# Optimization experiments

Hardware: AMD Instinct MI355X
Metric: run time of the kernel (lower is better)

## Reference

```python
import jax, jax.numpy as jnp
import numpy as np

B, ND, NK = 4096, 32, 64        # batch, num_drones, num_docks
FD, FK = 16, 16                  # nfeat_drone, nfeat_dock
NHID, H = 128, 4                 # hidden dim, attention heads
ALPHA = 0.2                      # leaky relu slope
NEG = -9e15                      # masking constant from torch code


def setup_inputs() -> dict:
    key = jax.random.key(0)
    ks = jax.random.split(key, 13)
    s = 0.1
    obs = jax.random.normal(ks[0], (B, ND * FD + NK * FK + ND * NK), jnp.float32)
    return {
        "obs": obs,
        # DroneDockGAT params (per-head projections + additive attention vectors)
        "W_drone": jax.random.normal(ks[1], (H, FD, NHID), jnp.float32) * s,
        "W_dock": jax.random.normal(ks[2], (H, FK, NHID), jnp.float32) * s,
        "a_src": jax.random.normal(ks[3], (H, NHID), jnp.float32) * s,
        "a_dst": jax.random.normal(ks[4], (H, NHID), jnp.float32) * s,
        # critic: Linear(nhid*num_drones,64) -> ReLU -> Linear(64,1)
        "Wc1": jax.random.normal(ks[5], (NHID * ND, 64), jnp.float32) * s,
        "bc1": jnp.zeros((64,), jnp.float32),
        "Wc2": jax.random.normal(ks[6], (64, 1), jnp.float32) * s,
        "bc2": jnp.zeros((1,), jnp.float32),
        # actor heads
        "Wad": jax.random.normal(ks[7], (NHID, NHID), jnp.float32) * s,
        "bad": jnp.zeros((NHID,), jnp.float32),
        "Wak": jax.random.normal(ks[8], (NHID, NHID), jnp.float32) * s,
        "bak": jnp.zeros((NHID,), jnp.float32),
    }


def reference(obs, W_drone, W_dock, a_src, a_dst, Wc1, bc1, Wc2, bc2, Wad, bad, Wak, bak):
    sd, sk = ND * FD, NK * FK
    drone = obs[:, :sd].reshape(B, ND, FD)
    dock = obs[:, sd:sd + sk].reshape(B, NK, FK)
    adj = obs[:, sd + sk:].reshape(B, ND, NK)

    # per-head projections: [B, H, ND, NHID] / [B, H, NK, NHID]
    Whd = jnp.einsum('bnf,hfk->bhnk', drone, W_drone)
    Whk = jnp.einsum('bmf,hfk->bhmk', dock, W_dock)

    # additive GAT attention scores e[b,h,n,m]
    e = jax.nn.leaky_relu(
        jnp.einsum('bhnk,hk->bhn', Whd, a_src)[:, :, :, None]
        + jnp.einsum('bhmk,hk->bhm', Whk, a_dst)[:, :, None, :],
        ALPHA,
    )
    e = jnp.where(adj[:, None, :, :] > 0, e, NEG)
    attn = jax.nn.softmax(e, axis=-1)

    # head-averaged outputs with ELU
    h_drone = jax.nn.elu(jnp.einsum('bhnm,bhmk->bnk', attn, Whk) / H)  # [B, ND, NHID]
    h_dock = jax.nn.elu(Whk.mean(axis=1))                               # [B, NK, NHID]

    # critic
    values = jax.nn.relu(h_drone.reshape(B, -1) @ Wc1 + bc1) @ Wc2 + bc2  # [B, 1]

    # actor: masked drone-dock score matrix
    q = h_drone @ Wad + bad
    k = h_dock @ Wak + bak
    scores = jnp.einsum('bnk,bmk->bnm', q, k)
    logits = jnp.where(adj > 0, scores, NEG)  # [B, ND, NK]
    return values, logits
```

## Files before the change

kernel.cpp:

```cpp
#include <hip/hip_runtime.h>
#include <math.h>

#define OBSD 3584
#define NEGC -9e15f

typedef short short8 __attribute__((ext_vector_type(8)));
typedef float float4v __attribute__((ext_vector_type(4)));

#define WS_MT_S   0
#define WS_U_F    8192
#define WS_W_F    8320
#define WS_C0_F   8448
#define WS_AW_F   8452
#define WS_WDMT_S 17160
#define WS_WFT_S  19208
#define WS_WC1H_S 32768
#define WS_WC1L_S 294912
#define WS_HD_S   557056
#define WS_NEED_BYTES  1114112ull
#define WS_NEED2_BYTES 34668544ull

__device__ __forceinline__ float elu_f(float x) {
    return x > 0.f ? x : (__expf(x) - 1.f);
}
__device__ __forceinline__ short f2bf(float f) {
    union { float f; unsigned u; } v; v.f = f;
    unsigned u = v.u;
    unsigned r = (u + 0x7fffu + ((u >> 16) & 1u)) >> 16;
    return (short)r;
}
__device__ __forceinline__ float b2f(short s) {
    union { unsigned u; float f; } v; v.u = ((unsigned)(unsigned short)s) << 16;
    return v.f;
}
__device__ __forceinline__ unsigned pk2(float a, float b) {
    return (unsigned)(unsigned short)f2bf(a) | ((unsigned)(unsigned short)f2bf(b) << 16);
}

__global__ __launch_bounds__(256) void setup_fold(
    const float* __restrict__ W_drone, const float* __restrict__ W_dock,
    const float* __restrict__ a_src, const float* __restrict__ a_dst,
    const float* __restrict__ Wad, const float* __restrict__ Wak,
    const float* __restrict__ bad, const float* __restrict__ bak,
    float* __restrict__ wsf, short* __restrict__ wss)
{
    const int t = threadIdx.x, bi = blockIdx.x;
    if (bi < 16) {
        __shared__ float sa[32 * 132];
        __shared__ float sb[32 * 132];
        const int r0 = (bi >> 2) * 32, i0 = (bi & 3) * 32;
        #pragma unroll
        for (int qq = 0; qq < 4; ++qq) {
            int e = (t + 256 * qq) * 4;
            int r = e >> 7, cc = e & 127;
            *(float4*)&sa[r * 132 + cc] = *(const float4*)&Wad[(r0 + r) * 128 + cc];
            *(float4*)&sb[r * 132 + cc] = *(const float4*)&Wak[(i0 + r) * 128 + cc];
        }
        __syncthreads();
        int rr = (t >> 4) * 2, ii = (t & 15) * 2;
        float a00 = 0.f, a01 = 0.f, a10 = 0.f, a11 = 0.f;
        for (int c = 0; c < 128; ++c) {
            float x0 = sa[rr * 132 + c], x1 = sa[(rr + 1) * 132 + c];
            float y0 = sb[ii * 132 + c], y1 = sb[(ii + 1) * 132 + c];
            a00 += x0 * y0; a01 += x0 * y1; a10 += x1 * y0; a11 += x1 * y1;
        }
        wss[WS_MT_S + (i0 + ii) * 128 + (r0 + rr)]         = f2bf(a00);
        wss[WS_MT_S + (i0 + ii + 1) * 128 + (r0 + rr)]     = f2bf(a01);
        wss[WS_MT_S + (i0 + ii) * 128 + (r0 + rr + 1)]     = f2bf(a10);
        wss[WS_MT_S + (i0 + ii + 1) * 128 + (r0 + rr + 1)] = f2bf(a11);
    } else if (bi == 16) {
        if (t < 128) {
            float acc = 0.f;
            for (int c = 0; c < 128; ++c) acc += Wad[t * 128 + c] * bak[c];
            wsf[WS_U_F + t] = acc;
        } else {
            int j = t - 128;
            float acc = 0.f;
            for (int c = 0; c < 128; ++c) acc += Wak[j * 128 + c] * bad[c];
            wsf[WS_W_F + j] = acc;
        }
        if (t == 0) {
            float acc = 0.f;
            for (int c = 0; c < 128; ++c) acc += bad[c] * bak[c];
            wsf[WS_C0_F] = acc;
        }
    } else {
        if (t < 64) {
            int h = t >> 4, f = t & 15;
            const float* wrow = W_drone + h * 2048 + f * 128;
            const float* arow = a_src + h * 128;
            float acc = 0.f;
            for (int k = 0; k < 128; ++k) acc += wrow[k] * arow[k];
            wsf[WS_AW_F + t] = acc;
        } else if (t < 128) {
            int tt = t - 64;
            int h = tt >> 4, f = tt & 15;
            const float* wrow = W_dock + h * 2048 + f * 128;
            const float* arow = a_dst + h * 128;
            float acc = 0.f;
            for (int k = 0; k < 128; ++k) acc += wrow[k] * arow[k];
            wsf[WS_AW_F + 64 + tt] = acc;
        }
        for (int idx = t; idx < 2048; idx += 256) {
            int k2 = idx >> 4, f = idx & 15;
            float v = 0.25f * (W_dock[f * 128 + k2] + W_dock[2048 + f * 128 + k2]
                             + W_dock[4096 + f * 128 + k2] + W_dock[6144 + f * 128 + k2]);
            wss[WS_WDMT_S + k2 * 16 + f] = f2bf(v);
        }
        for (int idx = t; idx < 8192; idx += 256) {
            int k2 = idx >> 6, f64 = idx & 63;
            float v = W_dock[(f64 >> 4) * 2048 + (f64 & 15) * 128 + k2];
            wss[WS_WFT_S + k2 * 64 + f64] = f2bf(v);
        }
    }
}

__global__ __launch_bounds__(256) void setup_wc1(
    const float* __restrict__ Wc1,
    short* __restrict__ wc1h, short* __restrict__ wc1l)
{
    __shared__ float tile[64 * 68];
    const int t = threadIdx.x;
    const int k0 = blockIdx.x * 64;
    {
        int r = t >> 2, c0 = (t & 3) * 16;
        const float4* src = (const float4*)&Wc1[(size_t)(k0 + r) * 64 + c0];
        #pragma unroll
        for (int u = 0; u < 4; ++u)
            *(float4*)&tile[r * 68 + c0 + 4 * u] = src[u];
    }
    __syncthreads();
    {
        int col = t >> 2, kk0 = (t & 3) * 16;
        short hi[16], lo[16];
        #pragma unroll
        for (int j = 0; j < 16; ++j) {
            float v = tile[(kk0 + j) * 68 + col];
            hi[j] = f2bf(v);
            lo[j] = f2bf(v - b2f(hi[j]));
        }
        uint4* dh = (uint4*)(wc1h + (size_t)col * 4096 + k0 + kk0);
        uint4* dl = (uint4*)(wc1l + (size_t)col * 4096 + k0 + kk0);
        dh[0] = *(uint4*)&hi[0]; dh[1] = *(uint4*)&hi[8];
        dl[0] = *(uint4*)&lo[0]; dl[1] = *(uint4*)&lo[8];
    }
}

__global__ __launch_bounds__(256, 2) void k13_fused(
    const float* __restrict__ obs,
    const float* __restrict__ wsf, const short* __restrict__ wss,
    short* __restrict__ hdg,
    float* __restrict__ out_logits)
{
    __shared__ __align__(16) char sm[74240];
    short* sD     = (short*)(sm + 0);
    short* sK     = (short*)(sm + 1024);
    short* sAdj   = (short*)(sm + 3072);
    float* sAw    = (float*)(sm + 7680);
    float* sSrc   = (float*)(sm + 8192);
    float* sDst   = (float*)(sm + 8704);
    short* sAt    = (short*)(sm + 9728);
    short* sT     = (short*)(sm + 28160);
    short* sHd    = (short*)(sm + 32768);
    short* sWf    = (short*)(sm + 41472);
    short* dockRm = (short*)(sm + 0);
    float* suL    = (float*)(sm + 8192);
    float* swL    = (float*)(sm + 8320);
    float* uL     = (float*)(sm + 8704);
    float* wL     = (float*)(sm + 9216);
    short* hkS    = (short*)(sm + 9728);
    short* wdmTS  = (short*)(sm + 28160);
    short* t2S    = (short*)(sm + 32768);
    short* MtS    = (short*)(sm + 41472);

    const int t = threadIdx.x;
    const int b = blockIdx.x;
    const float* obsrow = obs + (size_t)b * OBSD;
    const int L = t & 63, c = L & 15, q = L >> 4, w = t >> 6;

    #pragma unroll
    for (int i = 0; i < 4; ++i) {
        int q4 = t + 256 * i;
        if (q4 < 896) {
            float4 v = ((const float4*)obsrow)[q4];
            int e0 = q4 * 4;
            if (e0 < 512) {
                int n = e0 >> 4, f0 = e0 & 15;
                sD[(f0 + 0) * 32 + n] = f2bf(v.x);
                sD[(f0 + 1) * 32 + n] = f2bf(v.y);
                sD[(f0 + 2) * 32 + n] = f2bf(v.z);
                sD[(f0 + 3) * 32 + n] = f2bf(v.w);
            } else if (e0 < 1536) {
                int e = e0 - 512;
                int m = e >> 4, f0 = e & 15;
                sK[(f0 + 0) * 64 + m] = f2bf(v.x);
                sK[(f0 + 1) * 64 + m] = f2bf(v.y);
                sK[(f0 + 2) * 64 + m] = f2bf(v.z);
                sK[(f0 + 3) * 64 + m] = f2bf(v.w);
            } else {
                int e = e0 - 1536;
                int n = e >> 6, m0 = e & 63;
                uint2 pkd = { pk2(v.x, v.y), pk2(v.z, v.w) };
                *(uint2*)&sAdj[n * 72 + m0] = pkd;
            }
        }
    }
    #pragma unroll
    for (int i = 0; i < 4; ++i)
        ((uint4*)sWf)[t + 256 * i] = ((const uint4*)(wss + WS_WFT_S))[t + 256 * i];
    if (t < 128) sAw[t] = wsf[WS_AW_F + t];
    __syncthreads();

    if (t < 128) {
        int h = t >> 5, n = t & 31;
        float acc = 0.f;
        #pragma unroll
        for (int f = 0; f < 16; ++f) acc += b2f(sD[f * 32 + n]) * sAw[h * 16 + f];
        sSrc[h * 32 + n] = acc;
    }
    {
        int h = t >> 6, m = t & 63;
        float acc = 0.f;
        #pragma unroll
        for (int f = 0; f < 16; ++f) acc += b2f(sK[f * 64 + m]) * sAw[64 + h * 16 + f];
        sDst[h * 64 + m] = acc;
    }
    __syncthreads();

    {
        int row = t >> 1, j = t & 1;
        int h = row >> 5, n = row & 31, m0 = j * 32;
        float sv = sSrc[h * 32 + n];
        float e32[32];
        float pmax = -INFINITY;
        #pragma unroll
        for (int mm = 0; mm < 32; ++mm) {
            int m = m0 + mm;
            float e = sv + sDst[h * 64 + m];
            e = e > 0.f ? e : 0.2f * e;
            e = (b2f(sAdj[n * 72 + m]) > 0.f) ? e : NEGC;
            e32[mm] = e;
            pmax = fmaxf(pmax, e);
        }
        pmax = fmaxf(pmax, __shfl_xor(pmax, 1, 2));
        float psum = 0.f;
        #pragma unroll
        for (int mm = 0; mm < 32; ++mm) { e32[mm] = __expf(e32[mm] - pmax); psum += e32[mm]; }
        psum += __shfl_xor(psum, 1, 2);
        float rinv = 1.f / psum;
        unsigned* ab = (unsigned*)sAt;
        int ub = (h * 2304 + n * 72 + m0) >> 1;
        #pragma unroll
        for (int mm = 0; mm < 32; mm += 2)
            ab[ub + (mm >> 1)] = pk2(e32[mm] * rinv, e32[mm + 1] * rinv);
    }
    __syncthreads();

    {
        int h = w;
        float4v accT[2] = { {0,0,0,0}, {0,0,0,0} };
        #pragma unroll
        for (int mt = 0; mt < 2; ++mt)
            #pragma unroll
            for (int kq = 0; kq < 2; ++kq) {
                short8 a = *(const short8*)&sAt[h * 2304 + (mt * 16 + c) * 72 + kq * 32 + q * 8];
                short8 bb = *(const short8*)&sK[c * 64 + kq * 32 + q * 8];
                accT[mt] = __builtin_amdgcn_mfma_f32_16x16x32_bf16(a, bb, accT[mt], 0, 0, 0);
            }
        #pragma unroll
        for (int mt = 0; mt < 2; ++mt)
            #pragma unroll
            for (int i = 0; i < 4; ++i)
                sT[(mt * 16 + q * 4 + i) * 72 + h * 16 + c] = f2bf(accT[mt][i]);
    }
    __syncthreads();

    {
        int mt = w & 1, ntb = (w >> 1) * 4;
        float4v acc[4] = { {0,0,0,0}, {0,0,0,0}, {0,0,0,0}, {0,0,0,0} };
        #pragma unroll
        for (int kq = 0; kq < 2; ++kq) {
            short8 a = *(const short8*)&sT[(mt * 16 + c) * 72 + kq * 32 + q * 8];
            #pragma unroll
            for (int p = 0; p < 4; ++p) {
                short8 bb = *(const short8*)&sWf[((ntb + p) * 16 + c) * 64 + kq * 32 + q * 8];
                acc[p] = __builtin_amdgcn_mfma_f32_16x16x32_bf16(a, bb, acc[p], 0, 0, 0);
            }
        }
        #pragma unroll
        for (int p = 0; p < 4; ++p)
            #pragma unroll
            for (int i = 0; i < 4; ++i) {
                float v = elu_f(acc[p][i] * 0.25f);
                sHd[(mt * 16 + q * 4 + i) * 136 + (ntb + p) * 16 + c] = f2bf(v);
            }
    }
    __syncthreads();

    {
        int n = t >> 3, k2 = (t & 7) * 16;
        uint4 x0 = *(const uint4*)&sHd[n * 136 + k2];
        uint4 x1 = *(const uint4*)&sHd[n * 136 + k2 + 8];
        uint4* dst = (uint4*)(hdg + (size_t)b * 4096 + n * 128 + k2);
        dst[0] = x0; dst[1] = x1;
    }
    {
        float4 v = ((const float4*)obsrow)[128 + t];
        int m = t >> 2, f0 = (t & 3) * 4;
        uint2 pkd = { pk2(v.x, v.y), pk2(v.z, v.w) };
        *(uint2*)&dockRm[m * 16 + f0] = pkd;
    }
    ((uint4*)wdmTS)[t] = ((const uint4*)(wss + WS_WDMT_S))[t];
    #pragma unroll
    for (int i = 0; i < 8; ++i)
        ((uint4*)MtS)[t + 256 * i] = ((const uint4*)(wss + WS_MT_S))[t + 256 * i];
    if (t < 128) uL[t] = wsf[WS_U_F + t];
    else wL[t - 128] = wsf[WS_W_F + (t - 128)];
    __syncthreads();

    {
        int mt = w;
        short8 a;
        if (q < 2) a = *(const short8*)&dockRm[(mt * 16 + c) * 16 + q * 8];
        else a = short8{0, 0, 0, 0, 0, 0, 0, 0};
        float swp[4] = {0.f, 0.f, 0.f, 0.f};
        #pragma unroll
        for (int nt = 0; nt < 8; ++nt) {
            short8 bb;
            if (q < 2) bb = *(const short8*)&wdmTS[(nt * 16 + c) * 16 + q * 8];
            else bb = short8{0, 0, 0, 0, 0, 0, 0, 0};
            float4v acc = {0, 0, 0, 0};
            acc = __builtin_amdgcn_mfma_f32_16x16x32_bf16(a, bb, acc, 0, 0, 0);
            float wv = wL[nt * 16 + c];
            #pragma unroll
            for (int i = 0; i < 4; ++i) {
                float ev = elu_f(acc[i]);
                hkS[(mt * 16 + q * 4 + i) * 136 + nt * 16 + c] = f2bf(ev);
                swp[i] += ev * wv;
            }
        }
        #pragma unroll
        for (int i = 0; i < 4; ++i) {
            float sv = swp[i];
            sv += __shfl_xor(sv, 1, 16);
            sv += __shfl_xor(sv, 2, 16);
            sv += __shfl_xor(sv, 4, 16);
            sv += __shfl_xor(sv, 8, 16);
            if (c == 0) swL[mt * 16 + q * 4 + i] = sv;
        }
    }
    {
        int n = t >> 3, p = t & 7;
        float a = 0.f;
        #pragma unroll
        for (int kk = 0; kk < 16; kk += 2) {
            unsigned uu = *(const unsigned*)&sHd[n * 136 + p * 16 + kk];
            a += b2f((short)(uu & 0xffff)) * uL[p * 16 + kk]
               + b2f((short)(uu >> 16))   * uL[p * 16 + kk + 1];
        }
        a += __shfl_xor(a, 1, 8);
        a += __shfl_xor(a, 2, 8);
        a += __shfl_xor(a, 4, 8);
        if (p == 0) suL[n] = a;
    }
    __syncthreads();

    {
        int mt = w & 1, ntb = (w >> 1) * 4;
        float4v acc[4] = { {0,0,0,0}, {0,0,0,0}, {0,0,0,0}, {0,0,0,0} };
        #pragma unroll
        for (int kq = 0; kq < 4; ++kq) {
            short8 a = *(const short8*)&sHd[(mt * 16 + c) * 136 + kq * 32 + q * 8];
            #pragma unroll
            for (int p = 0; p < 4; ++p) {
                short8 bb = *(const short8*)&MtS[((ntb + p) * 16 + c) * 128 + kq * 32 + q * 8];
                acc[p] = __builtin_amdgcn_mfma_f32_16x16x32_bf16(a, bb, acc[p], 0, 0, 0);
            }
        }
        __syncthreads();
        #pragma unroll
        for (int p = 0; p < 4; ++p)
            #pragma unroll
            for (int i = 0; i < 4; ++i)
                t2S[(mt * 16 + q * 4 + i) * 136 + (ntb + p) * 16 + c] = f2bf(acc[p][i]);
    }
    __syncthreads();

    {
        const float c0v = wsf[WS_C0_F];
        int ntd = w;
        float* lg = out_logits + (size_t)b * 2048;
        #pragma unroll
        for (int mt = 0; mt < 2; ++mt) {
            float4v acc = {0, 0, 0, 0};
            #pragma unroll
            for (int kq = 0; kq < 4; ++kq) {
                short8 a  = *(const short8*)&t2S[(mt * 16 + c) * 136 + kq * 32 + q * 8];
                short8 bb = *(const short8*)&hkS[(ntd * 16 + c) * 136 + kq * 32 + q * 8];
                acc = __builtin_amdgcn_mfma_f32_16x16x32_bf16(a, bb, acc, 0, 0, 0);
            }
            int col = ntd * 16 + c;
            float swv = swL[col];
            #pragma unroll
            for (int i = 0; i < 4; ++i) {
                int row = mt * 16 + q * 4 + i;
                float val = acc[i] + suL[row] + swv + c0v;
                bool keep = b2f(sAdj[row * 72 + col]) > 0.f;
                lg[row * 64 + col] = keep ? val : NEGC;
            }
        }
    }
}

__global__ __launch_bounds__(256, 2) void k1_attn_hd(
    const float* __restrict__ obs,
    const float* __restrict__ wsf, const short* __restrict__ wss,
    short* __restrict__ hdg)
{
    __shared__ __align__(16) char sm[57856];
    short* sD   = (short*)(sm + 0);
    short* sK   = (short*)(sm + 1024);
    short* sAdj = (short*)(sm + 3072);
    float* sAw  = (float*)(sm + 7680);
    float* sSrc = (float*)(sm + 8192);
    float* sDst = (float*)(sm + 8704);
    short* sAt  = (short*)(sm + 9728);
    short* sT   = (short*)(sm + 28160);
    short* sHd  = (short*)(sm + 32768);
    short* sWf  = (short*)(sm + 41472);

    const int t = threadIdx.x;
    const int b = blockIdx.x;
    const float* obsrow = obs + (size_t)b * OBSD;
    const int L = t & 63, c = L & 15, q = L >> 4, w = t >> 6;

    #pragma unroll
    for (int i = 0; i < 4; ++i) {
        int q4 = t + 256 * i;
        if (q4 < 896) {
            float4 v = ((const float4*)obsrow)[q4];
            int e0 = q4 * 4;
            if (e0 < 512) {
                int n = e0 >> 4, f0 = e0 & 15;
                sD[(f0 + 0) * 32 + n] = f2bf(v.x);
                sD[(f0 + 1) * 32 + n] = f2bf(v.y);
                sD[(f0 + 2) * 32 + n] = f2bf(v.z);
                sD[(f0 + 3) * 32 + n] = f2bf(v.w);
            } else if (e0 < 1536) {
                int e = e0 - 512;
                int m = e >> 4, f0 = e & 15;
                sK[(f0 + 0) * 64 + m] = f2bf(v.x);
                sK[(f0 + 1) * 64 + m] = f2bf(v.y);
                sK[(f0 + 2) * 64 + m] = f2bf(v.z);
                sK[(f0 + 3) * 64 + m] = f2bf(v.w);
            } else {
                int e = e0 - 1536;
                int n = e >> 6, m0 = e & 63;
                uint2 pkd = { pk2(v.x, v.y), pk2(v.z, v.w) };
                *(uint2*)&sAdj[n * 72 + m0] = pkd;
            }
        }
    }
    #pragma unroll
    for (int i = 0; i < 4; ++i)
        ((uint4*)sWf)[t + 256 * i] = ((const uint4*)(wss + WS_WFT_S))[t + 256 * i];
    if (t < 128) sAw[t] = wsf[WS_AW_F + t];
    __syncthreads();

    if (t < 128) {
        int h = t >> 5, n = t & 31;
        float acc = 0.f;
        #pragma unroll
        for (int f = 0; f < 16; ++f) acc += b2f(sD[f * 32 + n]) * sAw[h * 16 + f];
        sSrc[h * 32 + n] = acc;
    }
    {
        int h = t >> 6, m = t & 63;
        float acc = 0.f;
        #pragma unroll
        for (int f = 0; f < 16; ++f) acc += b2f(sK[f * 64 + m]) * sAw[64 + h * 16 + f];
        sDst[h * 64 + m] = acc;
    }
    __syncthreads();

    {
        int row = t >> 1, j = t & 1;
        int h = row >> 5, n = row & 31, m0 = j * 32;
        float sv = sSrc[h * 32 + n];
        float e32[32];
        float pmax = -INFINITY;
        #pragma unroll
        for (int mm = 0; mm < 32; ++mm) {
            int m = m0 + mm;
            float e = sv + sDst[h * 64 + m];
            e = e > 0.f ? e : 0.2f * e;
            e = (b2f(sAdj[n * 72 + m]) > 0.f) ? e : NEGC;
            e32[mm] = e;
            pmax = fmaxf(pmax, e);
        }
        pmax = fmaxf(pmax, __shfl_xor(pmax, 1, 2));
        float psum = 0.f;
        #pragma unroll
        for (int mm = 0; mm < 32; ++mm) { e32[mm] = __expf(e32[mm] - pmax); psum += e32[mm]; }
        psum += __shfl_xor(psum, 1, 2);
        float rinv = 1.f / psum;
        unsigned* ab = (unsigned*)sAt;
        int ub = (h * 2304 + n * 72 + m0) >> 1;
        #pragma unroll
        for (int mm = 0; mm < 32; mm += 2)
            ab[ub + (mm >> 1)] = pk2(e32[mm] * rinv, e32[mm + 1] * rinv);
    }
    __syncthreads();

    {
        int h = w;
        float4v accT[2] = { {0,0,0,0}, {0,0,0,0} };
        #pragma unroll
        for (int mt = 0; mt < 2; ++mt)
            #pragma unroll
            for (int kq = 0; kq < 2; ++kq) {
                short8 a = *(const short8*)&sAt[h * 2304 + (mt * 16 + c) * 72 + kq * 32 + q * 8];
                short8 bb = *(const short8*)&sK[c * 64 + kq * 32 + q * 8];
                accT[mt] = __builtin_amdgcn_mfma_f32_16x16x32_bf16(a, bb, accT[mt], 0, 0, 0);
            }
        #pragma unroll
        for (int mt = 0; mt < 2; ++mt)
            #pragma unroll
            for (int i = 0; i < 4; ++i)
                sT[(mt * 16 + q * 4 + i) * 72 + h * 16 + c] = f2bf(accT[mt][i]);
    }
    __syncthreads();

    {
        int mt = w & 1, ntb = (w >> 1) * 4;
        float4v acc[4] = { {0,0,0,0}, {0,0,0,0}, {0,0,0,0}, {0,0,0,0} };
        #pragma unroll
        for (int kq = 0; kq < 2; ++kq) {
            short8 a = *(const short8*)&sT[(mt * 16 + c) * 72 + kq * 32 + q * 8];
            #pragma unroll
            for (int p = 0; p < 4; ++p) {
                short8 bb = *(const short8*)&sWf[((ntb + p) * 16 + c) * 64 + kq * 32 + q * 8];
                acc[p] = __builtin_amdgcn_mfma_f32_16x16x32_bf16(a, bb, acc[p], 0, 0, 0);
            }
        }
        #pragma unroll
        for (int p = 0; p < 4; ++p)
            #pragma unroll
            for (int i = 0; i < 4; ++i) {
                float v = elu_f(acc[p][i] * 0.25f);
                sHd[(mt * 16 + q * 4 + i) * 136 + (ntb + p) * 16 + c] = f2bf(v);
            }
    }
    __syncthreads();

    {
        int n = t >> 3, k2 = (t & 7) * 16;
        uint4 x0 = *(const uint4*)&sHd[n * 136 + k2];
        uint4 x1 = *(const uint4*)&sHd[n * 136 + k2 + 8];
        uint4* dst = (uint4*)(hdg + (size_t)b * 4096 + n * 128 + k2);
        dst[0] = x0; dst[1] = x1;
    }
}

__global__ __launch_bounds__(256) void k2_critic(
    const short* __restrict__ hdg,
    const float* __restrict__ Wc1, const float* __restrict__ bc1,
    const float* __restrict__ Wc2, const float* __restrict__ bc2,
    float* __restrict__ out_values)
{
    __shared__ __align__(16) char sm[46592];
    short* As   = (short*)(sm + 0);
    float* Wst  = (float*)(sm + 9216);
    short* Bh   = (short*)(sm + 27648);
    short* Blo  = (short*)(sm + 36864);
    float* bc1L = (float*)(sm + 46080);
    float* wc2L = (float*)(sm + 46336);

    const int t = threadIdx.x;
    const int r0 = blockIdx.x * 64;
    const int L = t & 63, c = L & 15, q = L >> 4, w = t >> 6;

    if (t < 64) { bc1L[t] = bc1[t]; wc2L[t] = Wc2[t]; }

    float4v acc[4] = { {0,0,0,0}, {0,0,0,0}, {0,0,0,0}, {0,0,0,0} };

    for (int kc = 0; kc < 64; ++kc) {
        __syncthreads();
        {
            int r = t >> 2, kk0 = (t & 3) * 16;
            const uint4* src = (const uint4*)(hdg + (size_t)(r0 + r) * 4096 + kc * 64 + kk0);
            *(uint4*)&As[r * 72 + kk0]     = src[0];
            *(uint4*)&As[r * 72 + kk0 + 8] = src[1];
        }
        {
            int el = t >> 2, j0 = (t & 3) * 16;
            const float4* src = (const float4*)&Wc1[(size_t)(kc * 64 + el) * 64 + j0];
            #pragma unroll
            for (int u = 0; u < 4; ++u)
                *(float4*)&Wst[el * 72 + j0 + 4 * u] = src[u];
        }
        __syncthreads();
        {
            int j = t & 63, elb = (t >> 6) * 16;
            #pragma unroll
            for (int e = 0; e < 16; e += 2) {
                float v0 = Wst[(elb + e) * 72 + j];
                float v1 = Wst[(elb + e + 1) * 72 + j];
                short h0 = f2bf(v0), h1 = f2bf(v1);
                float l0 = v0 - b2f(h0), l1 = v1 - b2f(h1);
                *(unsigned*)&Bh[j * 72 + elb + e]  = (unsigned)(unsigned short)h0 | ((unsigned)(unsigned short)h1 << 16);
                *(unsigned*)&Blo[j * 72 + elb + e] = (unsigned)(unsigned short)f2bf(l0) | ((unsigned)(unsigned short)f2bf(l1) << 16);
            }
        }
        __syncthreads();
        #pragma unroll
        for (int kq = 0; kq < 2; ++kq) {
            short8 a = *(const short8*)&As[(w * 16 + c) * 72 + kq * 32 + q * 8];
            #pragma unroll
            for (int ct = 0; ct < 4; ++ct) {
                short8 bh = *(const short8*)&Bh[(ct * 16 + c) * 72 + kq * 32 + q * 8];
                short8 bl = *(const short8*)&Blo[(ct * 16 + c) * 72 + kq * 32 + q * 8];
                acc[ct] = __builtin_amdgcn_mfma_f32_16x16x32_bf16(a, bh, acc[ct], 0, 0, 0);
                acc[ct] = __builtin_amdgcn_mfma_f32_16x16x32_bf16(a, bl, acc[ct], 0, 0, 0);
            }
        }
    }
    float bc2v = bc2[0];
    #pragma unroll
    for (int i = 0; i < 4; ++i) {
        float sv = 0.f;
        #pragma unroll
        for (int ct = 0; ct < 4; ++ct) {
            float pre = acc[ct][i] + bc1L[ct * 16 + c];
            pre = fmaxf(pre, 0.f);
            sv += pre * wc2L[ct * 16 + c];
        }
        sv += __shfl_xor(sv, 1, 16);
        sv += __shfl_xor(sv, 2, 16);
        sv += __shfl_xor(sv, 4, 16);
        sv += __shfl_xor(sv, 8, 16);
        if (c == 0) out_values[r0 + w * 16 + q * 4 + i] = sv + bc2v;
    }
}

__global__ __launch_bounds__(256) void k2_critic2(
    const short* __restrict__ hdg,
    const short* __restrict__ wc1h, const short* __restrict__ wc1l,
    const float* __restrict__ bc1,
    const float* __restrict__ Wc2, const float* __restrict__ bc2,
    float* __restrict__ out_values)
{
    __shared__ __align__(16) char sm[39936];
    short* As   = (short*)(sm + 0);
    short* Bh   = (short*)(sm + 4352);
    short* Bl   = (short*)(sm + 21760);
    float* bc1L = (float*)(sm + 39168);
    float* wc2L = (float*)(sm + 39424);
    float* red  = (float*)(sm + 39680);

    const int t = threadIdx.x;
    const int r0 = blockIdx.x * 16;
    const int L = t & 63, c = L & 15, q = L >> 4, w = t >> 6;

    if (t < 64) { bc1L[t] = bc1[t]; wc2L[t] = Wc2[t]; }

    float4v acc = {0, 0, 0, 0};

    const int rA  = t >> 4,  kkA = (t & 15) * 8;
    const int colB = t >> 2, kbB = (t & 3) * 32;

    for (int it = 0; it < 32; ++it) {
        const int kc = it * 128;
        __syncthreads();
        *(uint4*)&As[rA * 136 + kkA] =
            *(const uint4*)(hdg + (size_t)(r0 + rA) * 4096 + kc + kkA);
        {
            const uint4* srcH = (const uint4*)(wc1h + (size_t)colB * 4096 + kc + kbB);
            const uint4* srcL = (const uint4*)(wc1l + (size_t)colB * 4096 + kc + kbB);
            #pragma unroll
            for (int u = 0; u < 4; ++u) {
                *(uint4*)&Bh[colB * 136 + kbB + 8 * u] = srcH[u];
                *(uint4*)&Bl[colB * 136 + kbB + 8 * u] = srcL[u];
            }
        }
        __syncthreads();
        #pragma unroll
        for (int kq = 0; kq < 4; ++kq) {
            short8 a  = *(const short8*)&As[c * 136 + kq * 32 + q * 8];
            short8 bh = *(const short8*)&Bh[(w * 16 + c) * 136 + kq * 32 + q * 8];
            short8 bl = *(const short8*)&Bl[(w * 16 + c) * 136 + kq * 32 + q * 8];
            acc = __builtin_amdgcn_mfma_f32_16x16x32_bf16(a, bh, acc, 0, 0, 0);
            acc = __builtin_amdgcn_mfma_f32_16x16x32_bf16(a, bl, acc, 0, 0, 0);
        }
    }
    #pragma unroll
    for (int i = 0; i < 4; ++i) {
        float pre = acc[i] + bc1L[w * 16 + c];
        pre = fmaxf(pre, 0.f);
        float sv = pre * wc2L[w * 16 + c];
        sv += __shfl_xor(sv, 1, 16);
        sv += __shfl_xor(sv, 2, 16);
        sv += __shfl_xor(sv, 4, 16);
        sv += __shfl_xor(sv, 8, 16);
        if (c == 0) red[w * 16 + q * 4 + i] = sv;
    }
    __syncthreads();
    if (t < 16) {
        float v = red[t] + red[16 + t] + red[32 + t] + red[48 + t] + bc2[0];
        out_values[r0 + t] = v;
    }
}

__global__ __launch_bounds__(256, 2) void k3_logits(
    const float* __restrict__ obs,
    const float* __restrict__ wsf, const short* __restrict__ wss,
    float* __restrict__ out_logits)
{
    __shared__ __align__(16) char sm[75648];
    short* dockRm = (short*)(sm + 0);
    short* adjBf  = (short*)(sm + 2048);
    short* hdS    = (short*)(sm + 6656);
    short* hkS    = (short*)(sm + 15360);
    short* wdmTS  = (short*)(sm + 32768);
    short* t2S    = (short*)(sm + 32768);
    float* suL    = (float*)(sm + 41472);
    float* swL    = (float*)(sm + 41600);
    float* uL     = (float*)(sm + 41856);
    float* wL     = (float*)(sm + 42368);
    short* MtS    = (short*)(sm + 42880);

    const int t = threadIdx.x;
    const int b = blockIdx.x;
    const float* obsrow = obs + (size_t)b * OBSD;
    short* hdg = (short*)out_logits;
    const int L = t & 63, c = L & 15, q = L >> 4, w = t >> 6;

    {
        int n = t >> 3, k2 = (t & 7) * 16;
        const uint4* src = (const uint4*)(hdg + (size_t)b * 4096 + n * 128 + k2);
        uint4 x0 = src[0], x1 = src[1];
        *(uint4*)&hdS[n * 136 + k2]     = x0;
        *(uint4*)&hdS[n * 136 + k2 + 8] = x1;
    }
    {
        float4 v = ((const float4*)obsrow)[128 + t];
        int m = t >> 2, f0 = (t & 3) * 4;
        uint2 pkd = { pk2(v.x, v.y), pk2(v.z, v.w) };
        *(uint2*)&dockRm[m * 16 + f0] = pkd;
    }
    #pragma unroll
    for (int i = 0; i < 2; ++i) {
        int q4 = 384 + t + 256 * i;
        if (q4 < 896) {
            float4 v = ((const float4*)obsrow)[q4];
            int e = q4 * 4 - 1536;
            int n = e >> 6, m0 = e & 63;
            uint2 pkd = { pk2(v.x, v.y), pk2(v.z, v.w) };
            *(uint2*)&adjBf[n * 72 + m0] = pkd;
        }
    }
    ((uint4*)wdmTS)[t] = ((const uint4*)(wss + WS_WDMT_S))[t];
    #pragma unroll
    for (int i = 0; i < 8; ++i)
        ((uint4*)MtS)[t + 256 * i] = ((const uint4*)(wss + WS_MT_S))[t + 256 * i];
    if (t < 128) uL[t] = wsf[WS_U_F + t];
    else wL[t - 128] = wsf[WS_W_F + (t - 128)];
    __syncthreads();

    {
        int mt = w;
        short8 a;
        if (q < 2) a = *(const short8*)&dockRm[(mt * 16 + c) * 16 + q * 8];
        else a = short8{0, 0, 0, 0, 0, 0, 0, 0};
        float swp[4] = {0.f, 0.f, 0.f, 0.f};
        #pragma unroll
        for (int nt = 0; nt < 8; ++nt) {
            short8 bb;
            if (q < 2) bb = *(const short8*)&wdmTS[(nt * 16 + c) * 16 + q * 8];
            else bb = short8{0, 0, 0, 0, 0, 0, 0, 0};
            float4v acc = {0, 0, 0, 0};
            acc = __builtin_amdgcn_mfma_f32_16x16x32_bf16(a, bb, acc, 0, 0, 0);
            float wv = wL[nt * 16 + c];
            #pragma unroll
            for (int i = 0; i < 4; ++i) {
                float ev = elu_f(acc[i]);
                hkS[(mt * 16 + q * 4 + i) * 136 + nt * 16 + c] = f2bf(ev);
                swp[i] += ev * wv;
            }
        }
        #pragma unroll
        for (int i = 0; i < 4; ++i) {
            float sv = swp[i];
            sv += __shfl_xor(sv, 1, 16);
            sv += __shfl_xor(sv, 2, 16);
            sv += __shfl_xor(sv, 4, 16);
            sv += __shfl_xor(sv, 8, 16);
            if (c == 0) swL[mt * 16 + q * 4 + i] = sv;
        }
    }
    {
        int n = t >> 3, p = t & 7;
        float a = 0.f;
        #pragma unroll
        for (int kk = 0; kk < 16; kk += 2) {
            unsigned uu = *(const unsigned*)&hdS[n * 136 + p * 16 + kk];
            a += b2f((short)(uu & 0xffff)) * uL[p * 16 + kk]
               + b2f((short)(uu >> 16))   * uL[p * 16 + kk + 1];
        }
        a += __shfl_xor(a, 1, 8);
        a += __shfl_xor(a, 2, 8);
        a += __shfl_xor(a, 4, 8);
        if (p == 0) suL[n] = a;
    }
    __syncthreads();

    {
        int mt = w & 1, ntb = (w >> 1) * 4;
        float4v acc[4] = { {0,0,0,0}, {0,0,0,0}, {0,0,0,0}, {0,0,0,0} };
        #pragma unroll
        for (int kq = 0; kq < 4; ++kq) {
            short8 a = *(const short8*)&hdS[(mt * 16 + c) * 136 + kq * 32 + q * 8];
            #pragma unroll
            for (int p = 0; p < 4; ++p) {
                short8 bb = *(const short8*)&MtS[((ntb + p) * 16 + c) * 128 + kq * 32 + q * 8];
                acc[p] = __builtin_amdgcn_mfma_f32_16x16x32_bf16(a, bb, acc[p], 0, 0, 0);
            }
        }
        __syncthreads();
        #pragma unroll
        for (int p = 0; p < 4; ++p)
            #pragma unroll
            for (int i = 0; i < 4; ++i)
                t2S[(mt * 16 + q * 4 + i) * 136 + (ntb + p) * 16 + c] = f2bf(acc[p][i]);
    }
    __syncthreads();

    {
        const float c0v = wsf[WS_C0_F];
        int ntd = w;
        float* lg = out_logits + (size_t)b * 2048;
        #pragma unroll
        for (int mt = 0; mt < 2; ++mt) {
            float4v acc = {0, 0, 0, 0};
            #pragma unroll
            for (int kq = 0; kq < 4; ++kq) {
                short8 a  = *(const short8*)&t2S[(mt * 16 + c) * 136 + kq * 32 + q * 8];
                short8 bb = *(const short8*)&hkS[(ntd * 16 + c) * 136 + kq * 32 + q * 8];
                acc = __builtin_amdgcn_mfma_f32_16x16x32_bf16(a, bb, acc, 0, 0, 0);
            }
            int col = ntd * 16 + c;
            float swv = swL[col];
            #pragma unroll
            for (int i = 0; i < 4; ++i) {
                int row = mt * 16 + q * 4 + i;
                float val = acc[i] + suL[row] + swv + c0v;
                bool keep = b2f(adjBf[row * 72 + col]) > 0.f;
                lg[row * 64 + col] = keep ? val : NEGC;
            }
        }
    }
}

extern "C" void kernel_launch(void* const* d_in, const int* in_sizes, int n_in,
                              void* d_out, int out_size, void* d_ws, size_t ws_size,
                              hipStream_t stream) {
    (void)in_sizes; (void)n_in; (void)out_size;
    const float* obs     = (const float*)d_in[0];
    const float* W_drone = (const float*)d_in[1];
    const float* W_dock  = (const float*)d_in[2];
    const float* a_src   = (const float*)d_in[3];
    const float* a_dst   = (const float*)d_in[4];
    const float* Wc1     = (const float*)d_in[5];
    const float* bc1     = (const float*)d_in[6];
    const float* Wc2     = (const float*)d_in[7];
    const float* bc2     = (const float*)d_in[8];
    const float* Wad     = (const float*)d_in[9];
    const float* bad     = (const float*)d_in[10];
    const float* Wak     = (const float*)d_in[11];
    const float* bak     = (const float*)d_in[12];
    float* out = (float*)d_out;
    float* wsf = (float*)d_ws;
    short* wss = (short*)d_ws;

    const bool ws_wc1 = (ws_size >= WS_NEED_BYTES);
    const bool ws_hd  = (ws_size >= WS_NEED2_BYTES);

    setup_fold<<<dim3(18), dim3(256), 0, stream>>>(
        W_drone, W_dock, a_src, a_dst, Wad, Wak, bad, bak, wsf, wss);
    if (ws_wc1)
        setup_wc1<<<dim3(64), dim3(256), 0, stream>>>(
            Wc1, wss + WS_WC1H_S, wss + WS_WC1L_S);

    if (ws_hd) {
        short* hdw = wss + WS_HD_S;
        k13_fused<<<dim3(4096), dim3(256), 0, stream>>>(
            obs, wsf, wss, hdw, out + 4096);
        k2_critic2<<<dim3(256), dim3(256), 0, stream>>>(
            hdw, wss + WS_WC1H_S, wss + WS_WC1L_S, bc1, Wc2, bc2, out);
    } else {
        short* hdg = (short*)(out + 4096);
        k1_attn_hd<<<dim3(4096), dim3(256), 0, stream>>>(obs, wsf, wss, hdg);
        if (ws_wc1)
            k2_critic2<<<dim3(256), dim3(256), 0, stream>>>(
                hdg, wss + WS_WC1H_S, wss + WS_WC1L_S, bc1, Wc2, bc2, out);
        else
            k2_critic<<<dim3(64), dim3(256), 0, stream>>>(hdg, Wc1, bc1, Wc2, bc2, out);
        k3_logits<<<dim3(4096), dim3(256), 0, stream>>>(obs, wsf, wss, out + 4096);
    }
}
```

Before: 248.1 us.

## Merge setup kernels and prefetch-pipeline critic GEMM over more blocks

Folds the separate Wc1 split/transpose kernel into the fold setup kernel, saving one launch. Replaces the critic kernel with a version that handles 8 rows per block (512 blocks instead of 256) and prefetches the next K-chunk into registers while the current chunk's MFMAs run. The A tile's upper 8 rows are zero-padded, so half of the MFMA work is wasted in exchange for twice the parallelism. The prefetch registers raise per-thread register use.

New measurement: 366.4 us. 1.48x slower.

```diff
diff --git a/kernel.cpp b/kernel.cpp
--- a/kernel.cpp
+++ b/kernel.cpp
@@ -37,17 +37,19 @@
     return (unsigned)(unsigned short)f2bf(a) | ((unsigned)(unsigned short)f2bf(b) << 16);
 }
 
-__global__ __launch_bounds__(256) void setup_fold(
+__global__ __launch_bounds__(256) void setup_all(
     const float* __restrict__ W_drone, const float* __restrict__ W_dock,
     const float* __restrict__ a_src, const float* __restrict__ a_dst,
     const float* __restrict__ Wad, const float* __restrict__ Wak,
     const float* __restrict__ bad, const float* __restrict__ bak,
-    float* __restrict__ wsf, short* __restrict__ wss)
+    const float* __restrict__ Wc1,
+    float* __restrict__ wsf, short* __restrict__ wss, int do_wc1)
 {
+    __shared__ __align__(16) char smu[33792];
     const int t = threadIdx.x, bi = blockIdx.x;
     if (bi < 16) {
-        __shared__ float sa[32 * 132];
-        __shared__ float sb[32 * 132];
+        float* sa = (float*)smu;
+        float* sb = (float*)(smu + 16896);
         const int r0 = (bi >> 2) * 32, i0 = (bi & 3) * 32;
         #pragma unroll
         for (int qq = 0; qq < 4; ++qq) {
@@ -84,7 +86,7 @@
             for (int c = 0; c < 128; ++c) acc += bad[c] * bak[c];
             wsf[WS_C0_F] = acc;
         }
-    } else {
+    } else if (bi == 17) {
         if (t < 64) {
             int h = t >> 4, f = t & 15;
             const float* wrow = W_drone + h * 2048 + f * 128;
@@ -112,37 +114,34 @@
             float v = W_dock[(f64 >> 4) * 2048 + (f64 & 15) * 128 + k2];
             wss[WS_WFT_S + k2 * 64 + f64] = f2bf(v);
         }
-    }
-}
-
-__global__ __launch_bounds__(256) void setup_wc1(
-    const float* __restrict__ Wc1,
-    short* __restrict__ wc1h, short* __restrict__ wc1l)
-{
-    __shared__ float tile[64 * 68];
-    const int t = threadIdx.x;
-    const int k0 = blockIdx.x * 64;
-    {
-        int r = t >> 2, c0 = (t & 3) * 16;
-        const float4* src = (const float4*)&Wc1[(size_t)(k0 + r) * 64 + c0];
-        #pragma unroll
-        for (int u = 0; u < 4; ++u)
-            *(float4*)&tile[r * 68 + c0 + 4 * u] = src[u];
-    }
-    __syncthreads();
-    {
-        int col = t >> 2, kk0 = (t & 3) * 16;
-        short hi[16], lo[16];
-        #pragma unroll
-        for (int j = 0; j < 16; ++j) {
-            float v = tile[(kk0 + j) * 68 + col];
-            hi[j] = f2bf(v);
-            lo[j] = f2bf(v - b2f(hi[j]));
-        }
-        uint4* dh = (uint4*)(wc1h + (size_t)col * 4096 + k0 + kk0);
-        uint4* dl = (uint4*)(wc1l + (size_t)col * 4096 + k0 + kk0);
-        dh[0] = *(uint4*)&hi[0]; dh[1] = *(uint4*)&hi[8];
-        dl[0] = *(uint4*)&lo[0]; dl[1] = *(uint4*)&lo[8];
+    } else {
+        if (!do_wc1) return;
+        float* tile = (float*)smu;
+        short* wc1h = wss + WS_WC1H_S;
+        short* wc1l = wss + WS_WC1L_S;
+        const int k0 = (bi - 18) * 64;
+        {
+            int r = t >> 2, c0 = (t & 3) * 16;
+            const float4* src = (const float4*)&Wc1[(size_t)(k0 + r) * 64 + c0];
+            #pragma unroll
+            for (int u = 0; u < 4; ++u)
+                *(float4*)&tile[r * 68 + c0 + 4 * u] = src[u];
+        }
+        __syncthreads();
+        {
+            int col = t >> 2, kk0 = (t & 3) * 16;
+            short hi[16], lo[16];
+            #pragma unroll
+            for (int j = 0; j < 16; ++j) {
+                float v = tile[(kk0 + j) * 68 + col];
+                hi[j] = f2bf(v);
+                lo[j] = f2bf(v - b2f(hi[j]));
+            }
+            uint4* dh = (uint4*)(wc1h + (size_t)col * 4096 + k0 + kk0);
+            uint4* dl = (uint4*)(wc1l + (size_t)col * 4096 + k0 + kk0);
+            dh[0] = *(uint4*)&hi[0]; dh[1] = *(uint4*)&hi[8];
+            dl[0] = *(uint4*)&lo[0]; dl[1] = *(uint4*)&lo[8];
+        }
     }
 }
 
@@ -412,6 +411,88 @@
     }
 }
 
+__global__ __launch_bounds__(256) void k2_critic3(
+    const short* __restrict__ hdg,
+    const short* __restrict__ wc1h, const short* __restrict__ wc1l,
+    const float* __restrict__ bc1,
+    const float* __restrict__ Wc2, const float* __restrict__ bc2,
+    float* __restrict__ out_values)
+{
+    __shared__ __align__(16) char sm[39936];
+    short* As   = (short*)(sm + 0);
+    short* Bh   = (short*)(sm + 4352);
+    short* Bl   = (short*)(sm + 21760);
+    float* bc1L = (float*)(sm + 39168);
+    float* wc2L = (float*)(sm + 39424);
+    float* red  = (float*)(sm + 39680);
+
+    const int t = threadIdx.x;
+    const int r0 = blockIdx.x * 8;
+    const int L = t & 63, c = L & 15, q = L >> 4, w = t >> 6;
+
+    if (t < 64) { bc1L[t] = bc1[t]; wc2L[t] = Wc2[t]; }
+    for (int idx = t; idx < 544; idx += 256)
+        ((unsigned*)(As + 8 * 136))[idx] = 0u;
+
+    const int rA  = t >> 4,  kkA = (t & 15) * 8;
+    const int colB = t >> 2, kbB = (t & 3) * 32;
+
+    uint4 pa;
+    uint4 pbh[4], pbl[4];
+    {
+        if (t < 128) pa = *(const uint4*)(hdg + (size_t)(r0 + rA) * 4096 + kkA);
+        const uint4* srcH = (const uint4*)(wc1h + (size_t)colB * 4096 + kbB);
+        const uint4* srcL = (const uint4*)(wc1l + (size_t)colB * 4096 + kbB);
+        #pragma unroll
+        for (int u = 0; u < 4; ++u) { pbh[u] = srcH[u]; pbl[u] = srcL[u]; }
+    }
+
+    float4v acc = {0, 0, 0, 0};
+
+    for (int it = 0; it < 32; ++it) {
+        __syncthreads();
+        if (t < 128) *(uint4*)&As[rA * 136 + kkA] = pa;
+        #pragma unroll
+        for (int u = 0; u < 4; ++u) {
+            *(uint4*)&Bh[colB * 136 + kbB + 8 * u] = pbh[u];
+            *(uint4*)&Bl[colB * 136 + kbB + 8 * u] = pbl[u];
+        }
+        __syncthreads();
+        if (it + 1 < 32) {
+            const int kc = (it + 1) * 128;
+            if (t < 128) pa = *(const uint4*)(hdg + (size_t)(r0 + rA) * 4096 + kc + kkA);
+            const uint4* srcH = (const uint4*)(wc1h + (size_t)colB * 4096 + kc + kbB);
+            const uint4* srcL = (const uint4*)(wc1l + (size_t)colB * 4096 + kc + kbB);
+            #pragma unroll
+            for (int u = 0; u < 4; ++u) { pbh[u] = srcH[u]; pbl[u] = srcL[u]; }
+        }
+        #pragma unroll
+        for (int kq = 0; kq < 4; ++kq) {
+            short8 a  = *(const short8*)&As[c * 136 + kq * 32 + q * 8];
+            short8 bh = *(const short8*)&Bh[(w * 16 + c) * 136 + kq * 32 + q * 8];
+            short8 bl = *(const short8*)&Bl[(w * 16 + c) * 136 + kq * 32 + q * 8];
+            acc = __builtin_amdgcn_mfma_f32_16x16x32_bf16(a, bh, acc, 0, 0, 0);
+            acc = __builtin_amdgcn_mfma_f32_16x16x32_bf16(a, bl, acc, 0, 0, 0);
+        }
+    }
+    #pragma unroll
+    for (int i = 0; i < 4; ++i) {
+        float pre = acc[i] + bc1L[w * 16 + c];
+        pre = fmaxf(pre, 0.f);
+        float sv = pre * wc2L[w * 16 + c];
+        sv += __shfl_xor(sv, 1, 16);
+        sv += __shfl_xor(sv, 2, 16);
+        sv += __shfl_xor(sv, 4, 16);
+        sv += __shfl_xor(sv, 8, 16);
+        if (c == 0 && q < 2) red[w * 8 + q * 4 + i] = sv;
+    }
+    __syncthreads();
+    if (t < 8) {
+        float v = red[t] + red[8 + t] + red[16 + t] + red[24 + t] + bc2[0];
+        out_values[r0 + t] = v;
+    }
+}
+
 __global__ __launch_bounds__(256, 2) void k1_attn_hd(
     const float* __restrict__ obs,
     const float* __restrict__ wsf, const short* __restrict__ wss,
@@ -643,74 +724,6 @@
     }
 }
 
-__global__ __launch_bounds__(256) void k2_critic2(
-    const short* __restrict__ hdg,
-    const short* __restrict__ wc1h, const short* __restrict__ wc1l,
-    const float* __restrict__ bc1,
-    const float* __restrict__ Wc2, const float* __restrict__ bc2,
-    float* __restrict__ out_values)
-{
-    __shared__ __align__(16) char sm[39936];
-    short* As   = (short*)(sm + 0);
-    short* Bh   = (short*)(sm + 4352);
-    short* Bl   = (short*)(sm + 21760);
-    float* bc1L = (float*)(sm + 39168);
-    float* wc2L = (float*)(sm + 39424);
-    float* red  = (float*)(sm + 39680);
-
-    const int t = threadIdx.x;
-    const int r0 = blockIdx.x * 16;
-    const int L = t & 63, c = L & 15, q = L >> 4, w = t >> 6;
-
-    if (t < 64) { bc1L[t] = bc1[t]; wc2L[t] = Wc2[t]; }
-
-    float4v acc = {0, 0, 0, 0};
-
-    const int rA  = t >> 4,  kkA = (t & 15) * 8;
-    const int colB = t >> 2, kbB = (t & 3) * 32;
-
-    for (int it = 0; it < 32; ++it) {
-        const int kc = it * 128;
-        __syncthreads();
-        *(uint4*)&As[rA * 136 + kkA] =
-            *(const uint4*)(hdg + (size_t)(r0 + rA) * 4096 + kc + kkA);
-        {
-            const uint4* srcH = (const uint4*)(wc1h + (size_t)colB * 4096 + kc + kbB);
-            const uint4* srcL = (const uint4*)(wc1l + (size_t)colB * 4096 + kc + kbB);
-            #pragma unroll
-            for (int u = 0; u < 4; ++u) {
-                *(uint4*)&Bh[colB * 136 + kbB + 8 * u] = srcH[u];
-                *(uint4*)&Bl[colB * 136 + kbB + 8 * u] = srcL[u];
-            }
-        }
-        __syncthreads();
-        #pragma unroll
-        for (int kq = 0; kq < 4; ++kq) {
-            short8 a  = *(const short8*)&As[c * 136 + kq * 32 + q * 8];
-            short8 bh = *(const short8*)&Bh[(w * 16 + c) * 136 + kq * 32 + q * 8];
-            short8 bl = *(const short8*)&Bl[(w * 16 + c) * 136 + kq * 32 + q * 8];
-            acc = __builtin_amdgcn_mfma_f32_16x16x32_bf16(a, bh, acc, 0, 0, 0);
-            acc = __builtin_amdgcn_mfma_f32_16x16x32_bf16(a, bl, acc, 0, 0, 0);
-        }
-    }
-    #pragma unroll
-    for (int i = 0; i < 4; ++i) {
-        float pre = acc[i] + bc1L[w * 16 + c];
-        pre = fmaxf(pre, 0.f);
-        float sv = pre * wc2L[w * 16 + c];
-        sv += __shfl_xor(sv, 1, 16);
-        sv += __shfl_xor(sv, 2, 16);
-        sv += __shfl_xor(sv, 4, 16);
-        sv += __shfl_xor(sv, 8, 16);
-        if (c == 0) red[w * 16 + q * 4 + i] = sv;
-    }
-    __syncthreads();
-    if (t < 16) {
-        float v = red[t] + red[16 + t] + red[32 + t] + red[48 + t] + bc2[0];
-        out_values[r0 + t] = v;
-    }
-}
-
 __global__ __launch_bounds__(256, 2) void k3_logits(
     const float* __restrict__ obs,
     const float* __restrict__ wsf, const short* __restrict__ wss,
@@ -885,23 +898,21 @@
     const bool ws_wc1 = (ws_size >= WS_NEED_BYTES);
     const bool ws_hd  = (ws_size >= WS_NEED2_BYTES);
 
-    setup_fold<<<dim3(18), dim3(256), 0, stream>>>(
-        W_drone, W_dock, a_src, a_dst, Wad, Wak, bad, bak, wsf, wss);
-    if (ws_wc1)
-        setup_wc1<<<dim3(64), dim3(256), 0, stream>>>(
-            Wc1, wss + WS_WC1H_S, wss + WS_WC1L_S);
+    setup_all<<<dim3(82), dim3(256), 0, stream>>>(
+        W_drone, W_dock, a_src, a_dst, Wad, Wak, bad, bak, Wc1,
+        wsf, wss, ws_wc1 ? 1 : 0);
 
     if (ws_hd) {
         short* hdw = wss + WS_HD_S;
         k13_fused<<<dim3(4096), dim3(256), 0, stream>>>(
             obs, wsf, wss, hdw, out + 4096);
-        k2_critic2<<<dim3(256), dim3(256), 0, stream>>>(
+        k2_critic3<<<dim3(512), dim3(256), 0, stream>>>(
             hdw, wss + WS_WC1H_S, wss + WS_WC1L_S, bc1, Wc2, bc2, out);
     } else {
         short* hdg = (short*)(out + 4096);
         k1_attn_hd<<<dim3(4096), dim3(256), 0, stream>>>(obs, wsf, wss, hdg);
         if (ws_wc1)
-            k2_critic2<<<dim3(256), dim3(256), 0, stream>>>(
+            k2_critic3<<<dim3(512), dim3(256), 0, stream>>>(
                 hdg, wss + WS_WC1H_S, wss + WS_WC1L_S, bc1, Wc2, bc2, out);
         else
             k2_critic<<<dim3(64), dim3(256), 0, stream>>>(hdg, Wc1, bc1, Wc2, bc2, out);
```
